# Kernel optimization log

Measured on AMD Instinct MI355X. Metric: run time of the kernel, lower is better.

The kernel has to match this reference:

```python
import jax, jax.numpy as jnp
import numpy as np

B, T, N, F = 16, 64, 5000, 1
E = 80000
HG, HT = 64, 128


def setup_inputs() -> dict:
    key = jax.random.key(0)
    ks = jax.random.split(key, 20)
    p = lambda i, shape: jax.random.normal(ks[i], shape, jnp.float32) * 0.05
    return {
        "x_seq": jax.random.normal(ks[0], (B, T, N, F), jnp.float32),
        "edge_index": jax.random.randint(ks[1], (2, E), 0, N, jnp.int64 if jax.config.jax_enable_x64 else jnp.int32),
        # SAGEConv 1: out = mean_agg(x_j) @ Wl + b + x_i @ Wr  (PyG lin_l has bias, lin_r none)
        "s1_Wl": p(2, (F, HG)), "s1_Wr": p(3, (F, HG)), "s1_b": jnp.zeros((HG,), jnp.float32),
        "s2_Wl": p(4, (HG, HG)), "s2_Wr": p(5, (HG, HG)), "s2_b": jnp.zeros((HG,), jnp.float32),
        # GRU (torch layout): W_ih [3H, in], W_hh [3H, H], gates ordered r,z,n
        "gru_Wih": p(6, (3 * HT, HG)), "gru_Whh": p(7, (3 * HT, HT)),
        "gru_bih": jnp.zeros((3 * HT,), jnp.float32), "gru_bhh": jnp.zeros((3 * HT,), jnp.float32),
        # head: Linear(HT,64) -> ReLU -> Linear(64,1)
        "h1_W": p(8, (HT, 64)), "h1_b": jnp.zeros((64,), jnp.float32),
        "h2_W": p(9, (64, 1)), "h2_b": jnp.zeros((1,), jnp.float32),
    }


def reference(x_seq, edge_index, s1_Wl, s1_Wr, s1_b, s2_Wl, s2_Wr, s2_b,
              gru_Wih, gru_Whh, gru_bih, gru_bhh, h1_W, h1_b, h2_W, h2_b):
    src, dst = edge_index[0], edge_index[1]
    # in-degree for mean aggregation (clamped to 1 like PyG mean aggr)
    deg = jax.ops.segment_sum(jnp.ones(src.shape, jnp.float32), dst, num_segments=N)
    inv_deg = (1.0 / jnp.maximum(deg, 1.0))[:, None]  # [N,1]

    def sage(x, Wl, Wr, b):  # x: [B, N, d]
        msg = x[:, src]  # gather source features: [B, E, d]
        agg = jax.vmap(lambda m: jax.ops.segment_sum(m, dst, num_segments=N))(msg)
        agg = agg * inv_deg  # mean over incoming edges
        return agg @ Wl + x @ Wr + b

    def conv_step(_, x_t):  # x_t: [B, N, F]
        h = jax.nn.relu(sage(x_t, s1_Wl, s1_Wr, s1_b))
        h = jax.nn.relu(sage(h, s2_Wl, s2_Wr, s2_b))
        return None, h.mean(axis=1)  # global mean pool -> [B, HG]

    _, outs = jax.lax.scan(conv_step, None, jnp.moveaxis(x_seq, 1, 0))  # [T, B, HG]

    def gru_step(h, x_t):  # h: [B, HT], x_t: [B, HG]
        gi = x_t @ gru_Wih.T + gru_bih
        gh = h @ gru_Whh.T + gru_bhh
        ir, iz, i_n = jnp.split(gi, 3, axis=-1)
        hr, hz, hn = jnp.split(gh, 3, axis=-1)
        r = jax.nn.sigmoid(ir + hr)
        z = jax.nn.sigmoid(iz + hz)
        n = jnp.tanh(i_n + r * hn)
        h_new = (1.0 - z) * n + z * h
        return h_new, None

    h0 = jnp.zeros((x_seq.shape[0], HT), x_seq.dtype)
    hT, _ = jax.lax.scan(gru_step, h0, outs)  # last hidden state == H[:, -1, :]

    out = jax.nn.relu(hT @ h1_W + h1_b) @ h2_W + h2_b  # [B, 1]
    return out[:, 0]
```

## Files before the change

kernel.cpp:

```cpp
#include <hip/hip_runtime.h>

#define NN 5000
#define EE 80000
#define BB 16
#define TT 64

constexpr int ECAP = 1216;

typedef float  f32x2 __attribute__((ext_vector_type(2)));
typedef float  f32x4 __attribute__((ext_vector_type(4)));
typedef short  short8 __attribute__((ext_vector_type(8)));

__device__ inline unsigned short f2bf(float f) {
  unsigned int u = __builtin_bit_cast(unsigned int, f);
  u = (u + 0x7fffu + ((u >> 16) & 1u)) >> 16;
  return (unsigned short)u;
}
__device__ inline float bf2f(unsigned short h) {
  unsigned int u = ((unsigned int)h) << 16;
  return __builtin_bit_cast(float, u);
}
__device__ inline unsigned int cvtpk(float lo, float hi) {
  unsigned int r;
  asm("v_cvt_pk_bf16_f32 %0, %1, %2" : "=v"(r) : "v"(lo), "v"(hi));
  return r;
}
__device__ inline int ebidx(int t) { return t + (t >> 5); }

__global__ void k_deg(const int* __restrict__ dst, int* __restrict__ deg) {
  int e = blockIdx.x * 256 + threadIdx.x;
  if (e < EE) atomicAdd(&deg[dst[e]], 1);
}

__global__ __launch_bounds__(1024) void k_sort(const int* __restrict__ deg,
                                               int* __restrict__ perm,
                                               int* __restrict__ rank) {
  __shared__ int hist[256];
  int t = threadIdx.x;
  if (t < 256) hist[t] = 0;
  __syncthreads();
  for (int n = t; n < NN; n += 1024) atomicAdd(&hist[min(deg[n], 255)], 1);
  __syncthreads();
  if (t == 0) { int run = 0; for (int d = 0; d < 256; ++d) { int c = hist[d]; hist[d] = run; run += c; } }
  __syncthreads();
  for (int n = t; n < NN; n += 1024) {
    int d = min(deg[n], 255);
    int p = atomicAdd(&hist[d], 1);
    perm[p] = n;
    rank[n] = p;
  }
}

__global__ __launch_bounds__(1024) void k_scan(const int* __restrict__ deg,
                                               const int* __restrict__ perm,
                                               int* __restrict__ rowptrP,
                                               float* __restrict__ invdegP) {
  __shared__ int part[1024];
  int t = threadIdx.x;
  const int CH = 5;
  int base = t * CH;
  int cnt[CH];
  int s = 0;
  for (int i = 0; i < CH; ++i) {
    int idx = base + i;
    int d = (idx < NN) ? deg[perm[idx]] : 0;
    cnt[i] = d; s += d;
  }
  part[t] = s;
  __syncthreads();
  for (int off = 1; off < 1024; off <<= 1) {
    int v = (t >= off) ? part[t - off] : 0;
    __syncthreads();
    part[t] += v;
    __syncthreads();
  }
  int run = part[t] - s;
  for (int i = 0; i < CH; ++i) {
    int idx = base + i;
    if (idx < NN) {
      rowptrP[idx] = run;
      invdegP[idx] = 1.0f / fmaxf((float)cnt[i], 1.0f);
      run += cnt[i];
    }
  }
  if (t == 0) rowptrP[NN] = EE;
}

__global__ void k_fill(const int* __restrict__ src, const int* __restrict__ dst,
                       const int* __restrict__ rowptrP, const int* __restrict__ rank,
                       int* __restrict__ fill, int* __restrict__ col) {
  int e = blockIdx.x * 256 + threadIdx.x;
  if (e < EE) {
    int r = rank[dst[e]];
    int p = atomicAdd(&fill[r], 1);
    col[rowptrP[r] + p] = src[e];
  }
}

__global__ __launch_bounds__(256) void k_axp(const float* __restrict__ xseq,
                                             const int* __restrict__ rowptrP,
                                             const int* __restrict__ colg,
                                             const float* __restrict__ invdegP,
                                             const int* __restrict__ perm,
                                             float2* __restrict__ axp) {
  int q = blockIdx.x;
  __shared__ float xl[NN];
  const float* xs = xseq + (size_t)q * NN;
  for (int i = threadIdx.x; i < NN; i += 256) xl[i] = xs[i];
  __syncthreads();
  for (int ii = threadIdx.x; ii < NN; ii += 256) {
    int r0 = rowptrP[ii], r1 = rowptrP[ii + 1];
    float s = 0.f;
    for (int i = r0; i < r1; ++i) s += xl[colg[i]];
    int pn = perm[ii];
    axp[(size_t)q * NN + pn] = make_float2(s * invdegP[ii], xl[pn]);
  }
}

__global__ void k_wsplit(const float* __restrict__ Wl2, const float* __restrict__ Wr2,
                         unsigned short* __restrict__ Bfh, unsigned short* __restrict__ Bfl) {
  int t = blockIdx.x * 256 + threadIdx.x;
  if (t >= 16 * 64) return;
  int frag = t >> 6, lane = t & 63;
  int ks = frag >> 2, tn = frag & 3;
  int nlo = lane & 15, lg = lane >> 4;
  #pragma unroll
  for (int i = 0; i < 8; ++i) {
    int k = ks * 32 + lg * 8 + i;
    int n = tn * 16 + nlo;
    float v = (k < 64) ? Wl2[k * 64 + n] : Wr2[(k - 64) * 64 + n];
    unsigned short h = f2bf(v);
    unsigned short l = f2bf(v - bf2f(h));
    Bfh[(size_t)t * 8 + i] = h;
    Bfl[(size_t)t * 8 + i] = l;
  }
}

__global__ __launch_bounds__(256, 6) void k_conv2(const float2* __restrict__ axp,
    const int* __restrict__ rowptrP, const int* __restrict__ colg,
    const float* __restrict__ invdegP, const int* __restrict__ perm,
    const float* __restrict__ wl1, const float* __restrict__ wr1, const float* __restrict__ b1,
    const unsigned short* __restrict__ Bfh, const unsigned short* __restrict__ Bfl,
    const float* __restrict__ b2,
    float* __restrict__ outs)
{
  __shared__ __align__(16) unsigned int At[64 * 65];
  __shared__ __align__(16) float2 eb[ECAP + ECAP / 32 + 2];
  float* ps = (float*)At;
  const int q  = blockIdx.y;
  const int n0 = blockIdx.x * 64;
  const int tid = threadIdx.x;
  const int w = tid >> 6, lane = tid & 63;
  const float2* ax = axp + (size_t)q * NN;

  const int slot = n0 + lane;
  const int r0 = rowptrP[min(slot, NN)];
  const int r1 = rowptrP[min(slot + 1, NN)];
  const int e0 = __builtin_amdgcn_readfirstlane(rowptrP[n0]);
  const int e1 = __builtin_amdgcn_readfirstlane(rowptrP[min(n0 + 64, NN)]);
  const int eblk = e1 - e0;
  const bool fits = eblk <= ECAP;

  if (fits) {
    for (int i = tid; i < eblk; i += 256)
      eb[ebidx(i)] = ax[colg[e0 + i]];
  }
  __syncthreads();

  f32x2 wl2[8], wr2[8], bb2[8];
  {
    const float4* wl4 = (const float4*)(wl1 + 16 * w);
    const float4* wr4 = (const float4*)(wr1 + 16 * w);
    const float4* b4  = (const float4*)(b1  + 16 * w);
    #pragma unroll
    for (int j = 0; j < 4; ++j) {
      float4 a = wl4[j], b = wr4[j], c = b4[j];
      wl2[2*j] = {a.x, a.y}; wl2[2*j+1] = {a.z, a.w};
      wr2[2*j] = {b.x, b.y}; wr2[2*j+1] = {b.z, b.w};
      bb2[2*j] = {c.x, c.y}; bb2[2*j+1] = {c.z, c.w};
    }
  }
  f32x2 acc2[8];
  #pragma unroll
  for (int j = 0; j < 8; ++j) acc2[j] = {0.f, 0.f};
  const f32x2 zer2 = {0.f, 0.f};

  auto edge = [&](f32x2 ab) {
    #pragma unroll
    for (int j = 0; j < 8; ++j) {
      f32x2 z;
      asm("v_pk_fma_f32 %0, %1, %2, %3 op_sel:[1,0,0] op_sel_hi:[1,1,1]"
          : "=v"(z) : "v"(ab), "v"(wr2[j]), "v"(bb2[j]));
      asm("v_pk_fma_f32 %0, %1, %2, %3 op_sel:[0,0,0] op_sel_hi:[0,1,1]"
          : "=v"(z) : "v"(ab), "v"(wl2[j]), "v"(z));
      z = __builtin_elementwise_max(z, zer2);
      asm("v_pk_add_f32 %0, %1, %2" : "=v"(acc2[j]) : "v"(acc2[j]), "v"(z));
    }
  };

  const int dg = r1 - r0;
  if (fits) {
    const int i0 = r0 - e0;
    for (int e = 0; e < dg; ++e) {
      float2 ab = eb[ebidx(i0 + e)];
      edge((f32x2){ab.x, ab.y});
    }
  } else {
    const int* __restrict__ cp = colg + r0;
    for (int e = 0; e < dg; ++e) {
      float2 ab = ax[cp[e]];
      edge((f32x2){ab.x, ab.y});
    }
  }

  {
    const float iv = invdegP[min(slot, NN - 1)];
    const f32x2 iv2 = {iv, iv};
    #pragma unroll
    for (int j = 0; j < 8; ++j) {
      f32x2 a = acc2[j] * iv2;
      unsigned int H = cvtpk(a.x, a.y);
      float f0 = __builtin_bit_cast(float, H << 16);
      float f1 = __builtin_bit_cast(float, H & 0xffff0000u);
      unsigned int L = cvtpk(a.x - f0, a.y - f1);
      At[(16 * w + 2 * j + 0) * 65 + lane] = __builtin_amdgcn_perm(H, L, 0x05040100u);
      At[(16 * w + 2 * j + 1) * 65 + lane] = __builtin_amdgcn_perm(H, L, 0x07060302u);
    }
  }
  __syncthreads();

  const int nlo = lane & 15, lg = lane >> 4;
  const int gslot = n0 + w * 16 + nlo;
  const bool valid = gslot < NN;
  float2 own = make_float2(0.f, 0.f);
  if (valid) own = ax[perm[gslot]];
  f32x4 acc[4] = {{0.f,0.f,0.f,0.f},{0.f,0.f,0.f,0.f},{0.f,0.f,0.f,0.f},{0.f,0.f,0.f,0.f}};

  #pragma unroll 1
  for (int ks = 0; ks < 2; ++ks) {
    unsigned int u[8];
    #pragma unroll
    for (int i = 0; i < 8; ++i)
      u[i] = At[(ks * 32 + lg * 8 + i) * 65 + w * 16 + nlo];
    int4 ah, al;
    ah.x = __builtin_amdgcn_perm(u[1], u[0], 0x07060302u);
    ah.y = __builtin_amdgcn_perm(u[3], u[2], 0x07060302u);
    ah.z = __builtin_amdgcn_perm(u[5], u[4], 0x07060302u);
    ah.w = __builtin_amdgcn_perm(u[7], u[6], 0x07060302u);
    al.x = __builtin_amdgcn_perm(u[1], u[0], 0x05040100u);
    al.y = __builtin_amdgcn_perm(u[3], u[2], 0x05040100u);
    al.z = __builtin_amdgcn_perm(u[5], u[4], 0x05040100u);
    al.w = __builtin_amdgcn_perm(u[7], u[6], 0x05040100u);
    short8 ah8 = __builtin_bit_cast(short8, ah);
    short8 al8 = __builtin_bit_cast(short8, al);
    const short8* bh = (const short8*)(Bfh + (size_t)ks * 4 * 64 * 8);
    const short8* bl = (const short8*)(Bfl + (size_t)ks * 4 * 64 * 8);
    #pragma unroll
    for (int tn = 0; tn < 4; ++tn) {
      short8 bhv = bh[tn * 64 + lane];
      short8 blv = bl[tn * 64 + lane];
      acc[tn] = __builtin_amdgcn_mfma_f32_16x16x32_bf16(al8, bhv, acc[tn], 0, 0, 0);
      acc[tn] = __builtin_amdgcn_mfma_f32_16x16x32_bf16(ah8, blv, acc[tn], 0, 0, 0);
      acc[tn] = __builtin_amdgcn_mfma_f32_16x16x32_bf16(ah8, bhv, acc[tn], 0, 0, 0);
    }
  }

  #pragma unroll 1
  for (int ks = 2; ks < 4; ++ks) {
    const int kb = (ks - 2) * 32 + lg * 8;
    float4 wa0 = *(const float4*)(wl1 + kb), wa1 = *(const float4*)(wl1 + kb + 4);
    float4 wb0 = *(const float4*)(wr1 + kb), wb1 = *(const float4*)(wr1 + kb + 4);
    float4 bc0 = *(const float4*)(b1 + kb),  bc1 = *(const float4*)(b1 + kb + 4);
    float hv[8];
    hv[0] = fmaxf(fmaf(own.x, wa0.x, fmaf(own.y, wb0.x, bc0.x)), 0.f);
    hv[1] = fmaxf(fmaf(own.x, wa0.y, fmaf(own.y, wb0.y, bc0.y)), 0.f);
    hv[2] = fmaxf(fmaf(own.x, wa0.z, fmaf(own.y, wb0.z, bc0.z)), 0.f);
    hv[3] = fmaxf(fmaf(own.x, wa0.w, fmaf(own.y, wb0.w, bc0.w)), 0.f);
    hv[4] = fmaxf(fmaf(own.x, wa1.x, fmaf(own.y, wb1.x, bc1.x)), 0.f);
    hv[5] = fmaxf(fmaf(own.x, wa1.y, fmaf(own.y, wb1.y, bc1.y)), 0.f);
    hv[6] = fmaxf(fmaf(own.x, wa1.z, fmaf(own.y, wb1.z, bc1.z)), 0.f);
    hv[7] = fmaxf(fmaf(own.x, wa1.w, fmaf(own.y, wb1.w, bc1.w)), 0.f);
    int4 ah, al;
    #pragma unroll
    for (int p = 0; p < 4; ++p) {
      unsigned int H = cvtpk(hv[2*p], hv[2*p+1]);
      float f0 = __builtin_bit_cast(float, H << 16);
      float f1 = __builtin_bit_cast(float, H & 0xffff0000u);
      unsigned int L = cvtpk(hv[2*p] - f0, hv[2*p+1] - f1);
      ((unsigned int*)&ah)[p] = H;
      ((unsigned int*)&al)[p] = L;
    }
    short8 ah8 = __builtin_bit_cast(short8, ah);
    short8 al8 = __builtin_bit_cast(short8, al);
    const short8* bh = (const short8*)(Bfh + (size_t)ks * 4 * 64 * 8);
    const short8* bl = (const short8*)(Bfl + (size_t)ks * 4 * 64 * 8);
    #pragma unroll
    for (int tn = 0; tn < 4; ++tn) {
      short8 bhv = bh[tn * 64 + lane];
      short8 blv = bl[tn * 64 + lane];
      acc[tn] = __builtin_amdgcn_mfma_f32_16x16x32_bf16(al8, bhv, acc[tn], 0, 0, 0);
      acc[tn] = __builtin_amdgcn_mfma_f32_16x16x32_bf16(ah8, blv, acc[tn], 0, 0, 0);
      acc[tn] = __builtin_amdgcn_mfma_f32_16x16x32_bf16(ah8, bhv, acc[tn], 0, 0, 0);
    }
  }
  __syncthreads();

  #pragma unroll
  for (int tn = 0; tn < 4; ++tn) {
    const float bias = b2[tn * 16 + nlo];
    float s = 0.f;
    #pragma unroll
    for (int r = 0; r < 4; ++r) {
      int nslot = n0 + w * 16 + lg * 4 + r;
      float v = fmaxf(acc[tn][r] + bias, 0.f);
      if (nslot < NN) s += v;
    }
    s += __shfl_xor(s, 16, 64);
    s += __shfl_xor(s, 32, 64);
    if (lg == 0) ps[w * 64 + tn * 16 + nlo] = s;
  }
  __syncthreads();
  if (tid < 64) {
    float t = ps[tid] + ps[64 + tid] + ps[128 + tid] + ps[192 + tid];
    int b = q / TT, tt = q % TT;
    atomicAdd(&outs[((size_t)tt * BB + b) * 64 + tid], t);
  }
}

__global__ void k_T(const float* __restrict__ Wih, const float* __restrict__ Whh,
                    float* __restrict__ WihT, float* __restrict__ WhhT) {
  int id = blockIdx.x * 256 + threadIdx.x;
  if (id < 384 * 64)  { int r = id / 64;  int c = id % 64;  WihT[c * 384 + r] = Wih[id]; }
  if (id < 384 * 128) { int r = id / 128; int c = id % 128; WhhT[c * 384 + r] = Whh[id]; }
}

__global__ __launch_bounds__(384) void k_gi(const float* __restrict__ outs,
                                            const float* __restrict__ WihT,
                                            const float* __restrict__ bih,
                                            float* __restrict__ gi) {
  int g = blockIdx.x;
  __shared__ float xl[64];
  int r = threadIdx.x;
  if (r < 64) xl[r] = outs[(size_t)g * 64 + r] * (1.0f / (float)NN);
  __syncthreads();
  float acc = bih[r];
  #pragma unroll 8
  for (int c = 0; c < 64; ++c) acc = fmaf(WihT[c * 384 + r], xl[c], acc);
  gi[(size_t)g * 384 + r] = acc;
}

__global__ __launch_bounds__(384) void k_gru(const float* __restrict__ gi,
                                             const float* __restrict__ WhhT,
                                             const float* __restrict__ bhh,
                                             const float* __restrict__ h1W,
                                             const float* __restrict__ h1b,
                                             const float* __restrict__ h2W,
                                             const float* __restrict__ h2b,
                                             float* __restrict__ out) {
  int b = blockIdx.x, r = threadIdx.x;
  __shared__ float hl[128];
  __shared__ float ghl[384];
  __shared__ float t1l[64];
  float wreg[128];
  #pragma unroll
  for (int c = 0; c < 128; ++c) wreg[c] = WhhT[c * 384 + r];
  float bh = bhh[r];
  if (r < 128) hl[r] = 0.f;
  __syncthreads();
  for (int t = 0; t < TT; ++t) {
    float acc = bh;
    #pragma unroll
    for (int c = 0; c < 128; ++c) acc = fmaf(wreg[c], hl[c], acc);
    ghl[r] = acc;
    __syncthreads();
    if (r < 128) {
      const float* gio = gi + ((size_t)t * BB + b) * 384;
      float ir = gio[r], iz = gio[128 + r], inn = gio[256 + r];
      float hr = ghl[r], hz = ghl[128 + r], hn = ghl[256 + r];
      float rg = 1.f / (1.f + expf(-(ir + hr)));
      float zg = 1.f / (1.f + expf(-(iz + hz)));
      float ng = tanhf(inn + rg * hn);
      hl[r] = (1.f - zg) * ng + zg * hl[r];
    }
    __syncthreads();
  }
  if (r < 64) {
    float a = h1b[r];
    #pragma unroll
    for (int c = 0; c < 128; ++c) a = fmaf(hl[c], h1W[c * 64 + r], a);
    t1l[r] = fmaxf(a, 0.f);
  }
  __syncthreads();
  if (r == 0) {
    float o = h2b[0];
    for (int j = 0; j < 64; ++j) o = fmaf(t1l[j], h2W[j], o);
    out[b] = o;
  }
}

extern "C" void kernel_launch(void* const* d_in, const int* in_sizes, int n_in,
                              void* d_out, int out_size, void* d_ws, size_t ws_size,
                              hipStream_t stream) {
  const float* xseq = (const float*)d_in[0];
  const int*   ei   = (const int*)d_in[1];
  const float* s1Wl = (const float*)d_in[2];
  const float* s1Wr = (const float*)d_in[3];
  const float* s1b  = (const float*)d_in[4];
  const float* s2Wl = (const float*)d_in[5];
  const float* s2Wr = (const float*)d_in[6];
  const float* s2b  = (const float*)d_in[7];
  const float* gWih = (const float*)d_in[8];
  const float* gWhh = (const float*)d_in[9];
  const float* gbih = (const float*)d_in[10];
  const float* gbhh = (const float*)d_in[11];
  const float* h1W  = (const float*)d_in[12];
  const float* h1b  = (const float*)d_in[13];
  const float* h2W  = (const float*)d_in[14];
  const float* h2b  = (const float*)d_in[15];
  float* out = (float*)d_out;

  char* ws = (char*)d_ws;
  int*    deg     = (int*)(ws + 0);
  int*    fill    = (int*)(ws + 20480);
  float*  outs    = (float*)(ws + 40960);
  int*    rowptrP = (int*)(ws + 303104);
  float*  invdegP = (float*)(ws + 323584);
  int*    col     = (int*)(ws + 344064);
  int*    perm    = (int*)(ws + 664576);
  int*    rank    = (int*)(ws + 685056);
  float2* axp     = (float2*)(ws + 705536);
  float*  WihT    = (float*)(ws + 41665536);
  float*  WhhT    = (float*)(ws + 41763840);
  float*  gi      = (float*)(ws + 41960448);
  unsigned short* Bfh = (unsigned short*)(ws + 43533312);
  unsigned short* Bfl = (unsigned short*)(ws + 43549696);

  const int* srcI = ei;
  const int* dstI = ei + EE;

  hipMemsetAsync(d_ws, 0, 303104, stream);
  k_deg  <<<(EE + 255) / 256, 256, 0, stream>>>(dstI, deg);
  k_sort <<<1, 1024, 0, stream>>>(deg, perm, rank);
  k_scan <<<1, 1024, 0, stream>>>(deg, perm, rowptrP, invdegP);
  k_fill <<<(EE + 255) / 256, 256, 0, stream>>>(srcI, dstI, rowptrP, rank, fill, col);
  k_wsplit<<<4, 256, 0, stream>>>(s2Wl, s2Wr, Bfh, Bfl);
  k_axp  <<<BB * TT, 256, 0, stream>>>(xseq, rowptrP, col, invdegP, perm, axp);
  dim3 g2(79, BB * TT);
  k_conv2<<<g2, 256, 0, stream>>>(axp, rowptrP, col, invdegP, perm,
                                  s1Wl, s1Wr, s1b, Bfh, Bfl, s2b, outs);
  k_T    <<<192, 256, 0, stream>>>(gWih, gWhh, WihT, WhhT);
  k_gi   <<<BB * TT, 384, 0, stream>>>(outs, WihT, gbih, gi);
  k_gru  <<<BB, 384, 0, stream>>>(gi, WhhT, gbhh, h1W, h1b, h2W, h2b, out);
}
```

Baseline: 1.191 ms.

## Process two graph-time slices per conv2 block to share edge indices

Each k_conv2 block now handles two (batch,time) slices instead of one, halving the grid. The column-index loads and edge-list staging are shared across both slices, with their features packed into float4 in one aliased shared buffer. The edge loop accumulates both slices using compiler vector FMAs instead of inline packed asm. The cost is more registers (launch bounds drop to 5 waves), fewer blocks, and serialized per-slice MFMA phases with extra barriers.

```diff
diff --git a/kernel.cpp b/kernel.cpp
--- a/kernel.cpp
+++ b/kernel.cpp
@@ -25,7 +25,7 @@
   asm("v_cvt_pk_bf16_f32 %0, %1, %2" : "=v"(r) : "v"(lo), "v"(hi));
   return r;
 }
-__device__ inline int ebidx(int t) { return t + (t >> 5); }
+__device__ inline int eb4idx(int t) { return t + (t >> 4); }
 
 __global__ void k_deg(const int* __restrict__ dst, int* __restrict__ deg) {
   int e = blockIdx.x * 256 + threadIdx.x;
@@ -136,7 +136,7 @@
   }
 }
 
-__global__ __launch_bounds__(256, 6) void k_conv2(const float2* __restrict__ axp,
+__global__ __launch_bounds__(256, 5) void k_conv2(const float2* __restrict__ axp,
     const int* __restrict__ rowptrP, const int* __restrict__ colg,
     const float* __restrict__ invdegP, const int* __restrict__ perm,
     const float* __restrict__ wl1, const float* __restrict__ wr1, const float* __restrict__ b1,
@@ -144,14 +144,18 @@
     const float* __restrict__ b2,
     float* __restrict__ outs)
 {
-  __shared__ __align__(16) unsigned int At[64 * 65];
-  __shared__ __align__(16) float2 eb[ECAP + ECAP / 32 + 2];
-  float* ps = (float*)At;
-  const int q  = blockIdx.y;
+  __shared__ __align__(16) char smem[(ECAP + ECAP / 16 + 4) * 16];
+  float4*       eb4 = (float4*)smem;
+  unsigned int* At  = (unsigned int*)smem;
+  float*        ps  = (float*)smem;
+
+  const int qp = blockIdx.y;
+  const int q0 = 2 * qp, q1 = 2 * qp + 1;
   const int n0 = blockIdx.x * 64;
   const int tid = threadIdx.x;
   const int w = tid >> 6, lane = tid & 63;
-  const float2* ax = axp + (size_t)q * NN;
+  const float2* ax0 = axp + (size_t)q0 * NN;
+  const float2* ax1 = axp + (size_t)q1 * NN;
 
   const int slot = n0 + lane;
   const int r0 = rowptrP[min(slot, NN)];
@@ -162,8 +166,11 @@
   const bool fits = eblk <= ECAP;
 
   if (fits) {
-    for (int i = tid; i < eblk; i += 256)
-      eb[ebidx(i)] = ax[colg[e0 + i]];
+    for (int i = tid; i < eblk; i += 256) {
+      int c = colg[e0 + i];
+      float2 a0 = ax0[c], a1 = ax1[c];
+      eb4[eb4idx(i)] = make_float4(a0.x, a0.y, a1.x, a1.y);
+    }
   }
   __syncthreads();
 
@@ -180,51 +187,50 @@
       bb2[2*j] = {c.x, c.y}; bb2[2*j+1] = {c.z, c.w};
     }
   }
-  f32x2 acc2[8];
+  f32x2 acc2a[8], acc2b[8];
   #pragma unroll
-  for (int j = 0; j < 8; ++j) acc2[j] = {0.f, 0.f};
+  for (int j = 0; j < 8; ++j) { acc2a[j] = {0.f, 0.f}; acc2b[j] = {0.f, 0.f}; }
   const f32x2 zer2 = {0.f, 0.f};
 
-  auto edge = [&](f32x2 ab) {
+  auto bodyA = [&](float a, float x) {
+    f32x2 ca = {a, a}, cx = {x, x};
     #pragma unroll
     for (int j = 0; j < 8; ++j) {
-      f32x2 z;
-      asm("v_pk_fma_f32 %0, %1, %2, %3 op_sel:[1,0,0] op_sel_hi:[1,1,1]"
-          : "=v"(z) : "v"(ab), "v"(wr2[j]), "v"(bb2[j]));
-      asm("v_pk_fma_f32 %0, %1, %2, %3 op_sel:[0,0,0] op_sel_hi:[0,1,1]"
-          : "=v"(z) : "v"(ab), "v"(wl2[j]), "v"(z));
-      z = __builtin_elementwise_max(z, zer2);
-      asm("v_pk_add_f32 %0, %1, %2" : "=v"(acc2[j]) : "v"(acc2[j]), "v"(z));
+      f32x2 z = __builtin_elementwise_fma(ca, wl2[j],
+                __builtin_elementwise_fma(cx, wr2[j], bb2[j]));
+      acc2a[j] += __builtin_elementwise_max(z, zer2);
+    }
+  };
+  auto bodyB = [&](float a, float x) {
+    f32x2 ca = {a, a}, cx = {x, x};
+    #pragma unroll
+    for (int j = 0; j < 8; ++j) {
+      f32x2 z = __builtin_elementwise_fma(ca, wl2[j],
+                __builtin_elementwise_fma(cx, wr2[j], bb2[j]));
+      acc2b[j] += __builtin_elementwise_max(z, zer2);
     }
   };
 
   const int dg = r1 - r0;
   if (fits) {
     const int i0 = r0 - e0;
-    for (int e = 0; e < dg; ++e) {
-      float2 ab = eb[ebidx(i0 + e)];
-      edge((f32x2){ab.x, ab.y});
+    int e = 0;
+    for (; e + 1 < dg; e += 2) {
+      float4 v0 = eb4[eb4idx(i0 + e)];
+      float4 v1 = eb4[eb4idx(i0 + e + 1)];
+      bodyA(v0.x, v0.y); bodyB(v0.z, v0.w);
+      bodyA(v1.x, v1.y); bodyB(v1.z, v1.w);
+    }
+    if (e < dg) {
+      float4 v0 = eb4[eb4idx(i0 + e)];
+      bodyA(v0.x, v0.y); bodyB(v0.z, v0.w);
     }
   } else {
     const int* __restrict__ cp = colg + r0;
     for (int e = 0; e < dg; ++e) {
-      float2 ab = ax[cp[e]];
-      edge((f32x2){ab.x, ab.y});
-    }
-  }
-
-  {
-    const float iv = invdegP[min(slot, NN - 1)];
-    const f32x2 iv2 = {iv, iv};
-    #pragma unroll
-    for (int j = 0; j < 8; ++j) {
-      f32x2 a = acc2[j] * iv2;
-      unsigned int H = cvtpk(a.x, a.y);
-      float f0 = __builtin_bit_cast(float, H << 16);
-      float f1 = __builtin_bit_cast(float, H & 0xffff0000u);
-      unsigned int L = cvtpk(a.x - f0, a.y - f1);
-      At[(16 * w + 2 * j + 0) * 65 + lane] = __builtin_amdgcn_perm(H, L, 0x05040100u);
-      At[(16 * w + 2 * j + 1) * 65 + lane] = __builtin_amdgcn_perm(H, L, 0x07060302u);
+      int c = cp[e];
+      float2 a0 = ax0[c], a1 = ax1[c];
+      bodyA(a0.x, a0.y); bodyB(a1.x, a1.y);
     }
   }
   __syncthreads();
@@ -232,98 +238,124 @@
   const int nlo = lane & 15, lg = lane >> 4;
   const int gslot = n0 + w * 16 + nlo;
   const bool valid = gslot < NN;
-  float2 own = make_float2(0.f, 0.f);
-  if (valid) own = ax[perm[gslot]];
-  f32x4 acc[4] = {{0.f,0.f,0.f,0.f},{0.f,0.f,0.f,0.f},{0.f,0.f,0.f,0.f},{0.f,0.f,0.f,0.f}};
-
-  #pragma unroll 1
-  for (int ks = 0; ks < 2; ++ks) {
-    unsigned int u[8];
-    #pragma unroll
-    for (int i = 0; i < 8; ++i)
-      u[i] = At[(ks * 32 + lg * 8 + i) * 65 + w * 16 + nlo];
-    int4 ah, al;
-    ah.x = __builtin_amdgcn_perm(u[1], u[0], 0x07060302u);
-    ah.y = __builtin_amdgcn_perm(u[3], u[2], 0x07060302u);
-    ah.z = __builtin_amdgcn_perm(u[5], u[4], 0x07060302u);
-    ah.w = __builtin_amdgcn_perm(u[7], u[6], 0x07060302u);
-    al.x = __builtin_amdgcn_perm(u[1], u[0], 0x05040100u);
-    al.y = __builtin_amdgcn_perm(u[3], u[2], 0x05040100u);
-    al.z = __builtin_amdgcn_perm(u[5], u[4], 0x05040100u);
-    al.w = __builtin_amdgcn_perm(u[7], u[6], 0x05040100u);
-    short8 ah8 = __builtin_bit_cast(short8, ah);
-    short8 al8 = __builtin_bit_cast(short8, al);
-    const short8* bh = (const short8*)(Bfh + (size_t)ks * 4 * 64 * 8);
-    const short8* bl = (const short8*)(Bfl + (size_t)ks * 4 * 64 * 8);
+  const int pnode = valid ? perm[gslot] : 0;
+  const float iv = invdegP[min(slot, NN - 1)];
+
+  #pragma unroll
+  for (int qi = 0; qi < 2; ++qi) {
+    const f32x2* acc2 = qi ? acc2b : acc2a;
+    const float2* axq = qi ? ax1 : ax0;
+    const int     qq  = qi ? q1 : q0;
+
+    {
+      const f32x2 iv2 = {iv, iv};
+      #pragma unroll
+      for (int j = 0; j < 8; ++j) {
+        f32x2 a = acc2[j] * iv2;
+        unsigned int H = cvtpk(a.x, a.y);
+        float f0 = __builtin_bit_cast(float, H << 16);
+        float f1 = __builtin_bit_cast(float, H & 0xffff0000u);
+        unsigned int L = cvtpk(a.x - f0, a.y - f1);
+        At[(16 * w + 2 * j + 0) * 65 + lane] = __builtin_amdgcn_perm(H, L, 0x05040100u);
+        At[(16 * w + 2 * j + 1) * 65 + lane] = __builtin_amdgcn_perm(H, L, 0x07060302u);
+      }
+    }
+    __syncthreads();
+
+    float2 own = make_float2(0.f, 0.f);
+    if (valid) own = axq[pnode];
+    f32x4 acc[4] = {{0.f,0.f,0.f,0.f},{0.f,0.f,0.f,0.f},{0.f,0.f,0.f,0.f},{0.f,0.f,0.f,0.f}};
+
+    #pragma unroll 1
+    for (int ks = 0; ks < 2; ++ks) {
+      unsigned int u[8];
+      #pragma unroll
+      for (int i = 0; i < 8; ++i)
+        u[i] = At[(ks * 32 + lg * 8 + i) * 65 + w * 16 + nlo];
+      int4 ah, al;
+      ah.x = __builtin_amdgcn_perm(u[1], u[0], 0x07060302u);
+      ah.y = __builtin_amdgcn_perm(u[3], u[2], 0x07060302u);
+      ah.z = __builtin_amdgcn_perm(u[5], u[4], 0x07060302u);
+      ah.w = __builtin_amdgcn_perm(u[7], u[6], 0x07060302u);
+      al.x = __builtin_amdgcn_perm(u[1], u[0], 0x05040100u);
+      al.y = __builtin_amdgcn_perm(u[3], u[2], 0x05040100u);
+      al.z = __builtin_amdgcn_perm(u[5], u[4], 0x05040100u);
+      al.w = __builtin_amdgcn_perm(u[7], u[6], 0x05040100u);
+      short8 ah8 = __builtin_bit_cast(short8, ah);
+      short8 al8 = __builtin_bit_cast(short8, al);
+      const short8* bh = (const short8*)(Bfh + (size_t)ks * 4 * 64 * 8);
+      const short8* bl = (const short8*)(Bfl + (size_t)ks * 4 * 64 * 8);
+      #pragma unroll
+      for (int tn = 0; tn < 4; ++tn) {
+        short8 bhv = bh[tn * 64 + lane];
+        short8 blv = bl[tn * 64 + lane];
+        acc[tn] = __builtin_amdgcn_mfma_f32_16x16x32_bf16(al8, bhv, acc[tn], 0, 0, 0);
+        acc[tn] = __builtin_amdgcn_mfma_f32_16x16x32_bf16(ah8, blv, acc[tn], 0, 0, 0);
+        acc[tn] = __builtin_amdgcn_mfma_f32_16x16x32_bf16(ah8, bhv, acc[tn], 0, 0, 0);
+      }
+    }
+
+    #pragma unroll 1
+    for (int ks = 2; ks < 4; ++ks) {
+      const int kb = (ks - 2) * 32 + lg * 8;
+      float4 wa0 = *(const float4*)(wl1 + kb), wa1 = *(const float4*)(wl1 + kb + 4);
+      float4 wb0 = *(const float4*)(wr1 + kb), wb1 = *(const float4*)(wr1 + kb + 4);
+      float4 bc0 = *(const float4*)(b1 + kb),  bc1 = *(const float4*)(b1 + kb + 4);
+      float hv[8];
+      hv[0] = fmaxf(fmaf(own.x, wa0.x, fmaf(own.y, wb0.x, bc0.x)), 0.f);
+      hv[1] = fmaxf(fmaf(own.x, wa0.y, fmaf(own.y, wb0.y, bc0.y)), 0.f);
+      hv[2] = fmaxf(fmaf(own.x, wa0.z, fmaf(own.y, wb0.z, bc0.z)), 0.f);
+      hv[3] = fmaxf(fmaf(own.x, wa0.w, fmaf(own.y, wb0.w, bc0.w)), 0.f);
+      hv[4] = fmaxf(fmaf(own.x, wa1.x, fmaf(own.y, wb1.x, bc1.x)), 0.f);
+      hv[5] = fmaxf(fmaf(own.x, wa1.y, fmaf(own.y, wb1.y, bc1.y)), 0.f);
+      hv[6] = fmaxf(fmaf(own.x, wa1.z, fmaf(own.y, wb1.z, bc1.z)), 0.f);
+      hv[7] = fmaxf(fmaf(own.x, wa1.w, fmaf(own.y, wb1.w, bc1.w)), 0.f);
+      int4 ah, al;
+      #pragma unroll
+      for (int p = 0; p < 4; ++p) {
+        unsigned int H = cvtpk(hv[2*p], hv[2*p+1]);
+        float f0 = __builtin_bit_cast(float, H << 16);
+        float f1 = __builtin_bit_cast(float, H & 0xffff0000u);
+        unsigned int L = cvtpk(hv[2*p] - f0, hv[2*p+1] - f1);
+        ((unsigned int*)&ah)[p] = H;
+        ((unsigned int*)&al)[p] = L;
+      }
+      short8 ah8 = __builtin_bit_cast(short8, ah);
+      short8 al8 = __builtin_bit_cast(short8, al);
+      const short8* bh = (const short8*)(Bfh + (size_t)ks * 4 * 64 * 8);
+      const short8* bl = (const short8*)(Bfl + (size_t)ks * 4 * 64 * 8);
+      #pragma unroll
+      for (int tn = 0; tn < 4; ++tn) {
+        short8 bhv = bh[tn * 64 + lane];
+        short8 blv = bl[tn * 64 + lane];
+        acc[tn] = __builtin_amdgcn_mfma_f32_16x16x32_bf16(al8, bhv, acc[tn], 0, 0, 0);
+        acc[tn] = __builtin_amdgcn_mfma_f32_16x16x32_bf16(ah8, blv, acc[tn], 0, 0, 0);
+        acc[tn] = __builtin_amdgcn_mfma_f32_16x16x32_bf16(ah8, bhv, acc[tn], 0, 0, 0);
+      }
+    }
+    __syncthreads();
+
     #pragma unroll
     for (int tn = 0; tn < 4; ++tn) {
-      short8 bhv = bh[tn * 64 + lane];
-      short8 blv = bl[tn * 64 + lane];
-      acc[tn] = __builtin_amdgcn_mfma_f32_16x16x32_bf16(al8, bhv, acc[tn], 0, 0, 0);
-      acc[tn] = __builtin_amdgcn_mfma_f32_16x16x32_bf16(ah8, blv, acc[tn], 0, 0, 0);
-      acc[tn] = __builtin_amdgcn_mfma_f32_16x16x32_bf16(ah8, bhv, acc[tn], 0, 0, 0);
-    }
-  }
-
-  #pragma unroll 1
-  for (int ks = 2; ks < 4; ++ks) {
-    const int kb = (ks - 2) * 32 + lg * 8;
-    float4 wa0 = *(const float4*)(wl1 + kb), wa1 = *(const float4*)(wl1 + kb + 4);
-    float4 wb0 = *(const float4*)(wr1 + kb), wb1 = *(const float4*)(wr1 + kb + 4);
-    float4 bc0 = *(const float4*)(b1 + kb),  bc1 = *(const float4*)(b1 + kb + 4);
-    float hv[8];
-    hv[0] = fmaxf(fmaf(own.x, wa0.x, fmaf(own.y, wb0.x, bc0.x)), 0.f);
-    hv[1] = fmaxf(fmaf(own.x, wa0.y, fmaf(own.y, wb0.y, bc0.y)), 0.f);
-    hv[2] = fmaxf(fmaf(own.x, wa0.z, fmaf(own.y, wb0.z, bc0.z)), 0.f);
-    hv[3] = fmaxf(fmaf(own.x, wa0.w, fmaf(own.y, wb0.w, bc0.w)), 0.f);
-    hv[4] = fmaxf(fmaf(own.x, wa1.x, fmaf(own.y, wb1.x, bc1.x)), 0.f);
-    hv[5] = fmaxf(fmaf(own.x, wa1.y, fmaf(own.y, wb1.y, bc1.y)), 0.f);
-    hv[6] = fmaxf(fmaf(own.x, wa1.z, fmaf(own.y, wb1.z, bc1.z)), 0.f);
-    hv[7] = fmaxf(fmaf(own.x, wa1.w, fmaf(own.y, wb1.w, bc1.w)), 0.f);
-    int4 ah, al;
-    #pragma unroll
-    for (int p = 0; p < 4; ++p) {
-      unsigned int H = cvtpk(hv[2*p], hv[2*p+1]);
-      float f0 = __builtin_bit_cast(float, H << 16);
-      float f1 = __builtin_bit_cast(float, H & 0xffff0000u);
-      unsigned int L = cvtpk(hv[2*p] - f0, hv[2*p+1] - f1);
-      ((unsigned int*)&ah)[p] = H;
-      ((unsigned int*)&al)[p] = L;
-    }
-    short8 ah8 = __builtin_bit_cast(short8, ah);
-    short8 al8 = __builtin_bit_cast(short8, al);
-    const short8* bh = (const short8*)(Bfh + (size_t)ks * 4 * 64 * 8);
-    const short8* bl = (const short8*)(Bfl + (size_t)ks * 4 * 64 * 8);
-    #pragma unroll
-    for (int tn = 0; tn < 4; ++tn) {
-      short8 bhv = bh[tn * 64 + lane];
-      short8 blv = bl[tn * 64 + lane];
-      acc[tn] = __builtin_amdgcn_mfma_f32_16x16x32_bf16(al8, bhv, acc[tn], 0, 0, 0);
-      acc[tn] = __builtin_amdgcn_mfma_f32_16x16x32_bf16(ah8, blv, acc[tn], 0, 0, 0);
-      acc[tn] = __builtin_amdgcn_mfma_f32_16x16x32_bf16(ah8, bhv, acc[tn], 0, 0, 0);
-    }
-  }
-  __syncthreads();
-
-  #pragma unroll
-  for (int tn = 0; tn < 4; ++tn) {
-    const float bias = b2[tn * 16 + nlo];
-    float s = 0.f;
-    #pragma unroll
-    for (int r = 0; r < 4; ++r) {
-      int nslot = n0 + w * 16 + lg * 4 + r;
-      float v = fmaxf(acc[tn][r] + bias, 0.f);
-      if (nslot < NN) s += v;
-    }
-    s += __shfl_xor(s, 16, 64);
-    s += __shfl_xor(s, 32, 64);
-    if (lg == 0) ps[w * 64 + tn * 16 + nlo] = s;
-  }
-  __syncthreads();
-  if (tid < 64) {
-    float t = ps[tid] + ps[64 + tid] + ps[128 + tid] + ps[192 + tid];
-    int b = q / TT, tt = q % TT;
-    atomicAdd(&outs[((size_t)tt * BB + b) * 64 + tid], t);
+      const float bias = b2[tn * 16 + nlo];
+      float s = 0.f;
+      #pragma unroll
+      for (int r = 0; r < 4; ++r) {
+        int nslot = n0 + w * 16 + lg * 4 + r;
+        float v = fmaxf(acc[tn][r] + bias, 0.f);
+        if (nslot < NN) s += v;
+      }
+      s += __shfl_xor(s, 16, 64);
+      s += __shfl_xor(s, 32, 64);
+      if (lg == 0) ps[w * 64 + tn * 16 + nlo] = s;
+    }
+    __syncthreads();
+    if (tid < 64) {
+      float t = ps[tid] + ps[64 + tid] + ps[128 + tid] + ps[192 + tid];
+      int b = qq / TT, tt = qq % TT;
+      atomicAdd(&outs[((size_t)tt * BB + b) * 64 + tid], t);
+    }
+    __syncthreads();
   }
 }
 
@@ -445,7 +477,7 @@
   k_fill <<<(EE + 255) / 256, 256, 0, stream>>>(srcI, dstI, rowptrP, rank, fill, col);
   k_wsplit<<<4, 256, 0, stream>>>(s2Wl, s2Wr, Bfh, Bfl);
   k_axp  <<<BB * TT, 256, 0, stream>>>(xseq, rowptrP, col, invdegP, perm, axp);
-  dim3 g2(79, BB * TT);
+  dim3 g2(79, BB * TT / 2);
   k_conv2<<<g2, 256, 0, stream>>>(axp, rowptrP, col, invdegP, perm,
                                   s1Wl, s1Wr, s1b, Bfh, Bfl, s2b, outs);
   k_T    <<<192, 256, 0, stream>>>(gWih, gWhh, WihT, WhhT);
```

Measured after the change: 1.123 ms (median of 2 runs). -5.7%, faster.
